# Kernel tuning notes

Hardware: AMD Instinct MI355X
Metric: run time of the kernel (lower is better)

## Reference

```python
import jax, jax.numpy as jnp
import numpy as np

B, N, INDIM, OUTDIM = 32, 128, 32, 64


def setup_inputs() -> dict:
    key = jax.random.key(0)
    k1, k2, k3, k4, k5, k6 = jax.random.split(key, 6)
    X = jax.random.normal(k1, (B, N, N, INDIM), dtype=jnp.float32)
    # variable subgraph sizes (irregular masking), at least 1 node per graph
    n_nodes = jnp.clip(jax.random.randint(k2, (B,), 0, N), 1, N).astype(jnp.int64)
    # MLP params (Linear + ReLU tail activation) for lin1 and lin2
    s = 1.0 / np.sqrt(INDIM)
    W1 = jax.random.uniform(k3, (INDIM, OUTDIM), jnp.float32, -s, s)
    b1 = jax.random.uniform(k4, (OUTDIM,), jnp.float32, -s, s)
    W2 = jax.random.uniform(k5, (INDIM, OUTDIM), jnp.float32, -s, s)
    b2 = jax.random.uniform(k6, (OUTDIM,), jnp.float32, -s, s)
    return {"X": X, "W1": W1, "b1": b1, "W2": W2, "b2": b2, "n_nodes": n_nodes}


def reference(X, W1, b1, W2, b2, n_nodes):
    # pairwise mask [B,N,N,1] from per-graph node counts (MaskedTensor mode 'DD')
    nm = jnp.arange(N)[None, :] < n_nodes[:, None]          # [B,N] node mask
    mask = (nm[:, :, None] & nm[:, None, :])[..., None].astype(X.dtype)  # [B,N,N,1]
    # tuplewiseapply of lin1 / lin2 (Linear + ReLU), zero-fill masked tuples
    X1 = jax.nn.relu(jnp.einsum('bijd,de->bije', X, W1) + b1) * mask  # [B,N,N,OUTDIM]
    X2 = jax.nn.relu(jnp.einsum('bijd,de->bije', X, W2) + b2) * mask
    # Op2FWL (aggr='sum'): per-channel batched matmul over node dim k
    out = jnp.einsum('bike,bkje->bije', X1, X2) * mask
    return out
```

## Files before the change

### kernel.cpp

```cpp
#include <hip/hip_runtime.h>

typedef unsigned short ushort_t;
typedef __attribute__((ext_vector_type(8))) __bf16 bf16x8;
typedef __attribute__((ext_vector_type(4))) float f32x4;


__device__ __forceinline__ ushort_t f32_to_bf16(float v) {
    unsigned ui = __float_as_uint(v);
    ui += 0x7fffu + ((ui >> 16) & 1u);
    return (ushort_t)(ui >> 16);
}

union FragU { bf16x8 f; ushort_t u[8]; };
union Pack4 { ushort_t us[4]; uint2 v; };

__global__ __launch_bounds__(256) void lin_mfma_kernel(
        const float* __restrict__ X,
        const float* __restrict__ W1, const float* __restrict__ b1v,
        const float* __restrict__ W2, const float* __restrict__ b2v,
        const int* __restrict__ n_nodes,
        ushort_t* __restrict__ X1t, ushort_t* __restrict__ X2t) {
    __shared__ ushort_t sO[64 * 136];
    const int blk = blockIdx.x;
    const int pass = blk >> 10;
    const int idx = blk & 1023;
    const int b = idx >> 5, rg = idx & 31;
    const int n = n_nodes[b];
    if (rg * 4 >= n) return;

    const float* W    = pass ? W2  : W1;
    const float* bias = pass ? b2v : b1v;
    ushort_t* Out     = pass ? X2t : X1t;
    const int rstride = pass ? 32 : 4096;
    const int tstride = pass ? 4096 : 32;

    const int u = threadIdx.x;
    const int w = u >> 6, l = u & 63;
    const int quad = l >> 4, lid = l & 15;

    FragU bfrag[4];
    float bia[4];
    #pragma unroll
    for (int ni = 0; ni < 4; ++ni) {
        const int e = ni * 16 + lid;
        #pragma unroll
        for (int j = 0; j < 8; ++j)
            bfrag[ni].u[j] = f32_to_bf16(W[(quad * 8 + j) * 64 + e]);
        bia[ni] = bias[e];
    }

    for (int q = 0; q < 4; ++q) {
        const int r = rg * 4 + q;
        if (r >= n) break;
        {
            const float* Xb = X + (size_t)b * 524288 + (size_t)r * rstride;
            #pragma unroll
            for (int s = 0; s < 2; ++s) {
                const int mt = w * 2 + s;
                const int t0b = mt * 16 + quad * 4;
                if (mt * 16 < n) {
                    const int m = mt * 16 + lid;
                    const float* xr = Xb + (size_t)m * tstride + quad * 8;
                    float4 x0 = *(const float4*)xr;
                    float4 x1 = *(const float4*)(xr + 4);
                    FragU af;
                    af.u[0] = f32_to_bf16(x0.x); af.u[1] = f32_to_bf16(x0.y);
                    af.u[2] = f32_to_bf16(x0.z); af.u[3] = f32_to_bf16(x0.w);
                    af.u[4] = f32_to_bf16(x1.x); af.u[5] = f32_to_bf16(x1.y);
                    af.u[6] = f32_to_bf16(x1.z); af.u[7] = f32_to_bf16(x1.w);
                    #pragma unroll
                    for (int ni = 0; ni < 4; ++ni) {
                        f32x4 acc = {};
                        acc = __builtin_amdgcn_mfma_f32_16x16x32_bf16(
                            af.f, bfrag[ni].f, acc, 0, 0, 0);
                        const int e = ni * 16 + lid;
                        Pack4 pk;
                        #pragma unroll
                        for (int rgi = 0; rgi < 4; ++rgi) {
                            const int t = t0b + rgi;
                            float v = (t < n) ? fmaxf(acc[rgi] + bia[ni], 0.f) : 0.f;
                            pk.us[rgi] = f32_to_bf16(v);
                        }
                        *(uint2*)(sO + e * 136 + t0b) = pk.v;
                    }
                } else {
                    Pack4 pk; pk.us[0] = pk.us[1] = pk.us[2] = pk.us[3] = 0;
                    #pragma unroll
                    for (int ni = 0; ni < 4; ++ni)
                        *(uint2*)(sO + (ni * 16 + lid) * 136 + t0b) = pk.v;
                }
            }
        }
        __syncthreads();
        {
            const int e = u >> 2, part = u & 3;
            if (part * 32 < n) {
                ushort_t* gO = Out + ((size_t)(b * 64 + e) * 128 + r) * 128 + part * 32;
                const ushort_t* sRow = sO + e * 136 + part * 32;
                #pragma unroll
                for (int c = 0; c < 4; ++c)
                    *(uint4*)(gO + c * 8) = *(const uint4*)(sRow + c * 8);
            }
        }
        __syncthreads();
    }
}

__global__ __launch_bounds__(256) void mm_kernel(
        const ushort_t* __restrict__ X1t, const ushort_t* __restrict__ X2t,
        ushort_t* __restrict__ Ct, const int* __restrict__ n_nodes) {
    __shared__ ushort_t sC[128 * 136];
    const int blk = blockIdx.x;
    const size_t plane = (size_t)blk * 16384;
    const int n = n_nodes[blk >> 6];
    const int kmax = (n + 31) & ~31;
    const ushort_t* Aj = X2t + plane;
    const ushort_t* Bi = X1t + plane;
    const int u = threadIdx.x;
    const int w = u >> 6, l = u & 63;
    const int quad = l >> 4, lid = l & 15;
    const int wj = (w >> 1) * 64, wi = (w & 1) * 64;
    const bool anyA = (wj < n), anyB = (wi < n);
    bool aAct[4], bAct[4];
    #pragma unroll
    for (int mj = 0; mj < 4; ++mj) aAct[mj] = (wj + mj * 16) < n;
    #pragma unroll
    for (int ni = 0; ni < 4; ++ni) bAct[ni] = (wi + ni * 16) < n;
    f32x4 acc[4][4] = {};

    for (int k0 = 0; k0 < kmax; k0 += 32) {
        bf16x8 af[4], bfr[4];
        #pragma unroll
        for (int mj = 0; mj < 4; ++mj)
            if (aAct[mj] && anyB)
                af[mj] = *(const bf16x8*)(Aj + (size_t)(wj + mj * 16 + lid) * 128 + k0 + quad * 8);
        #pragma unroll
        for (int ni = 0; ni < 4; ++ni)
            if (bAct[ni] && anyA)
                bfr[ni] = *(const bf16x8*)(Bi + (size_t)(wi + ni * 16 + lid) * 128 + k0 + quad * 8);
        #pragma unroll
        for (int mj = 0; mj < 4; ++mj)
            #pragma unroll
            for (int ni = 0; ni < 4; ++ni)
                if (aAct[mj] && bAct[ni])
                    acc[mj][ni] = __builtin_amdgcn_mfma_f32_16x16x32_bf16(
                        af[mj], bfr[ni], acc[mj][ni], 0, 0, 0);
    }

    #pragma unroll
    for (int mj = 0; mj < 4; ++mj)
        #pragma unroll
        for (int ni = 0; ni < 4; ++ni) {
            const int j0 = wj + mj * 16 + quad * 4;
            const int i  = wi + ni * 16 + lid;
            Pack4 pk;
            #pragma unroll
            for (int rg = 0; rg < 4; ++rg)
                pk.us[rg] = f32_to_bf16(acc[mj][ni][rg]);
            *(uint2*)(sC + i * 136 + j0) = pk.v;
        }
    __syncthreads();
    ushort_t* Cp = Ct + plane;
    #pragma unroll
    for (int it = 0; it < 8; ++it) {
        int idx = it * 256 + u;
        int i = idx >> 4, c = idx & 15;
        if (i < n && c * 8 < n)
            *(uint4*)(Cp + (size_t)idx * 8) = *(const uint4*)(sC + i * 136 + c * 8);
    }
}

__global__ __launch_bounds__(256) void tr_kernel(
        const ushort_t* __restrict__ Ct, float* __restrict__ out,
        const int* __restrict__ n_nodes) {
    __shared__ float sT[64 * 129];
    const int blk = blockIdx.x;
    const int b = blk >> 7, i = blk & 127;
    const int u = threadIdx.x;
    const int n = n_nodes[b];
    float* ob = out + ((size_t)b * 16384 + (size_t)i * 128) * 64;

    if (i >= n) {
        float4 z = {0.f, 0.f, 0.f, 0.f};
        #pragma unroll
        for (int it = 0; it < 8; ++it)
            *(float4*)(ob + (size_t)(it * 256 + u) * 4) = z;
        return;
    }

    const ushort_t* Cb = Ct + (size_t)b * 1048576 + (size_t)i * 128;
    #pragma unroll
    for (int it = 0; it < 4; ++it) {
        int idx = it * 256 + u;
        int e = idx >> 4, c = idx & 15;
        float* dst = sT + e * 129 + c * 8;
        const int rem = n - c * 8;
        if (rem >= 8) {
            uint4 v = *(const uint4*)(Cb + (size_t)e * 16384 + c * 8);
            dst[0] = __uint_as_float(v.x << 16);
            dst[1] = __uint_as_float(v.x & 0xffff0000u);
            dst[2] = __uint_as_float(v.y << 16);
            dst[3] = __uint_as_float(v.y & 0xffff0000u);
            dst[4] = __uint_as_float(v.z << 16);
            dst[5] = __uint_as_float(v.z & 0xffff0000u);
            dst[6] = __uint_as_float(v.w << 16);
            dst[7] = __uint_as_float(v.w & 0xffff0000u);
        } else if (rem > 0) {
            uint4 v = *(const uint4*)(Cb + (size_t)e * 16384 + c * 8);
            float tmp[8];
            tmp[0] = __uint_as_float(v.x << 16);
            tmp[1] = __uint_as_float(v.x & 0xffff0000u);
            tmp[2] = __uint_as_float(v.y << 16);
            tmp[3] = __uint_as_float(v.y & 0xffff0000u);
            tmp[4] = __uint_as_float(v.z << 16);
            tmp[5] = __uint_as_float(v.z & 0xffff0000u);
            tmp[6] = __uint_as_float(v.w << 16);
            tmp[7] = __uint_as_float(v.w & 0xffff0000u);
            #pragma unroll
            for (int t = 0; t < 8; ++t) dst[t] = (t < rem) ? tmp[t] : 0.f;
        } else {
            #pragma unroll
            for (int t = 0; t < 8; ++t) dst[t] = 0.f;
        }
    }
    __syncthreads();

    #pragma unroll
    for (int it = 0; it < 8; ++it) {
        int idx = it * 256 + u;
        int j = idx >> 4, e0 = (idx & 15) * 4;
        float4 vv;
        vv.x = sT[(e0 + 0) * 129 + j];
        vv.y = sT[(e0 + 1) * 129 + j];
        vv.z = sT[(e0 + 2) * 129 + j];
        vv.w = sT[(e0 + 3) * 129 + j];
        *(float4*)(ob + (size_t)idx * 4) = vv;
    }
}

extern "C" void kernel_launch(void* const* d_in, const int* in_sizes, int n_in,
                              void* d_out, int out_size, void* d_ws, size_t ws_size,
                              hipStream_t stream) {
    const float* X  = (const float*)d_in[0];
    const float* W1 = (const float*)d_in[1];
    const float* b1 = (const float*)d_in[2];
    const float* W2 = (const float*)d_in[3];
    const float* b2 = (const float*)d_in[4];
    const int* nn   = (const int*)d_in[5];
    float* out = (float*)d_out;

    ushort_t* X1t = (ushort_t*)d_ws;
    ushort_t* X2t = X1t + 33554432;
    ushort_t* Ct  = X1t;

    lin_mfma_kernel<<<2048, 256, 0, stream>>>(X, W1, b1, W2, b2, nn, X1t, X2t);
    mm_kernel<<<2048, 256, 0, stream>>>(X1t, X2t, Ct, nn);
    tr_kernel<<<4096, 256, 0, stream>>>(Ct, out, nn);
}
```

Measured before the change: 268.1 us.

## Tile linear kernel over 32x32 (i,j) blocks, computing both projections from one X tile

The linear stage now assigns each block a 32x32 (i,j) tile and a half of the output channels. Each block computes both the X1 and X2 projections from the same X tile, writing X2 transposed through shared memory. Before, X was read twice with a strided access pattern for the X2 pass. The aim is to read X contiguously and reuse it across both projections, at the cost of each X tile being read by two channel-half blocks and of scalar-granularity transposed LDS stores.

```diff
diff --git a/kernel.cpp b/kernel.cpp
--- a/kernel.cpp
+++ b/kernel.cpp
@@ -14,92 +14,105 @@
 union FragU { bf16x8 f; ushort_t u[8]; };
 union Pack4 { ushort_t us[4]; uint2 v; };
 
-__global__ __launch_bounds__(256) void lin_mfma_kernel(
+#define SYP 1036
+
+__global__ __launch_bounds__(256) void lin2_kernel(
         const float* __restrict__ X,
         const float* __restrict__ W1, const float* __restrict__ b1v,
         const float* __restrict__ W2, const float* __restrict__ b2v,
         const int* __restrict__ n_nodes,
         ushort_t* __restrict__ X1t, ushort_t* __restrict__ X2t) {
-    __shared__ ushort_t sO[64 * 136];
+    __shared__ ushort_t sY[32 * SYP];
     const int blk = blockIdx.x;
-    const int pass = blk >> 10;
-    const int idx = blk & 1023;
-    const int b = idx >> 5, rg = idx & 31;
+    const int b  = blk >> 5;
+    const int eh = (blk >> 4) & 1;
+    const int it = (blk >> 2) & 3, jt = blk & 3;
+    const int i0 = it * 32, j0 = jt * 32;
     const int n = n_nodes[b];
-    if (rg * 4 >= n) return;
-
-    const float* W    = pass ? W2  : W1;
-    const float* bias = pass ? b2v : b1v;
-    ushort_t* Out     = pass ? X2t : X1t;
-    const int rstride = pass ? 32 : 4096;
-    const int tstride = pass ? 4096 : 32;
-
+    if (i0 >= n || j0 >= n) return;
     const int u = threadIdx.x;
     const int w = u >> 6, l = u & 63;
     const int quad = l >> 4, lid = l & 15;
-
-    FragU bfrag[4];
-    float bia[4];
-    #pragma unroll
-    for (int ni = 0; ni < 4; ++ni) {
-        const int e = ni * 16 + lid;
-        #pragma unroll
-        for (int j = 0; j < 8; ++j)
-            bfrag[ni].u[j] = f32_to_bf16(W[(quad * 8 + j) * 64 + e]);
-        bia[ni] = bias[e];
-    }
-
-    for (int q = 0; q < 4; ++q) {
-        const int r = rg * 4 + q;
-        if (r >= n) break;
-        {
-            const float* Xb = X + (size_t)b * 524288 + (size_t)r * rstride;
-            #pragma unroll
-            for (int s = 0; s < 2; ++s) {
-                const int mt = w * 2 + s;
-                const int t0b = mt * 16 + quad * 4;
-                if (mt * 16 < n) {
-                    const int m = mt * 16 + lid;
-                    const float* xr = Xb + (size_t)m * tstride + quad * 8;
-                    float4 x0 = *(const float4*)xr;
-                    float4 x1 = *(const float4*)(xr + 4);
-                    FragU af;
-                    af.u[0] = f32_to_bf16(x0.x); af.u[1] = f32_to_bf16(x0.y);
-                    af.u[2] = f32_to_bf16(x0.z); af.u[3] = f32_to_bf16(x0.w);
-                    af.u[4] = f32_to_bf16(x1.x); af.u[5] = f32_to_bf16(x1.y);
-                    af.u[6] = f32_to_bf16(x1.z); af.u[7] = f32_to_bf16(x1.w);
-                    #pragma unroll
-                    for (int ni = 0; ni < 4; ++ni) {
-                        f32x4 acc = {};
-                        acc = __builtin_amdgcn_mfma_f32_16x16x32_bf16(
-                            af.f, bfrag[ni].f, acc, 0, 0, 0);
-                        const int e = ni * 16 + lid;
+    const int e0 = eh * 32;
+    const float* Xb = X + (size_t)b * 524288;
+
+    for (int p = 0; p < 2; ++p) {
+        const float* W    = p ? W2  : W1;
+        const float* bias = p ? b2v : b1v;
+        ushort_t* Out     = p ? X2t : X1t;
+        const int r0 = p ? j0 : i0;
+        const int c0 = p ? i0 : j0;
+
+        FragU bfrag[2];
+        float bia[2];
+        #pragma unroll
+        for (int ni = 0; ni < 2; ++ni) {
+            const int e = e0 + ni * 16 + lid;
+            #pragma unroll
+            for (int jj = 0; jj < 8; ++jj)
+                bfrag[ni].u[jj] = f32_to_bf16(W[(quad * 8 + jj) * 64 + e]);
+            bia[ni] = bias[e];
+        }
+
+        for (int mm = 0; mm < 16; ++mm) {
+            const int mt = w * 16 + mm;
+            const int il = mt >> 1, jl0 = (mt & 1) * 16;
+            const int gi = i0 + il;
+            if (gi < n) {
+                const float* xr = Xb + (size_t)gi * 4096
+                                     + (size_t)(j0 + jl0 + lid) * 32 + quad * 8;
+                float4 x0 = *(const float4*)xr;
+                float4 x1 = *(const float4*)(xr + 4);
+                FragU af;
+                af.u[0] = f32_to_bf16(x0.x); af.u[1] = f32_to_bf16(x0.y);
+                af.u[2] = f32_to_bf16(x0.z); af.u[3] = f32_to_bf16(x0.w);
+                af.u[4] = f32_to_bf16(x1.x); af.u[5] = f32_to_bf16(x1.y);
+                af.u[6] = f32_to_bf16(x1.z); af.u[7] = f32_to_bf16(x1.w);
+                #pragma unroll
+                for (int ni = 0; ni < 2; ++ni) {
+                    f32x4 acc = {};
+                    acc = __builtin_amdgcn_mfma_f32_16x16x32_bf16(
+                        af.f, bfrag[ni].f, acc, 0, 0, 0);
+                    const int el = ni * 16 + lid;
+                    if (p == 0) {
                         Pack4 pk;
                         #pragma unroll
-                        for (int rgi = 0; rgi < 4; ++rgi) {
-                            const int t = t0b + rgi;
-                            float v = (t < n) ? fmaxf(acc[rgi] + bia[ni], 0.f) : 0.f;
-                            pk.us[rgi] = f32_to_bf16(v);
+                        for (int rg = 0; rg < 4; ++rg) {
+                            const int gj = j0 + jl0 + quad * 4 + rg;
+                            float v = (gj < n) ? fmaxf(acc[rg] + bia[ni], 0.f) : 0.f;
+                            pk.us[rg] = f32_to_bf16(v);
                         }
-                        *(uint2*)(sO + e * 136 + t0b) = pk.v;
+                        *(uint2*)(sY + el * SYP + il * 32 + jl0 + quad * 4) = pk.v;
+                    } else {
+                        #pragma unroll
+                        for (int rg = 0; rg < 4; ++rg) {
+                            const int jl = jl0 + quad * 4 + rg;
+                            float v = ((j0 + jl) < n) ? fmaxf(acc[rg] + bia[ni], 0.f) : 0.f;
+                            sY[el * SYP + jl * 32 + il] = f32_to_bf16(v);
+                        }
                     }
-                } else {
-                    Pack4 pk; pk.us[0] = pk.us[1] = pk.us[2] = pk.us[3] = 0;
+                }
+            } else if (p == 1) {
+                #pragma unroll
+                for (int ni = 0; ni < 2; ++ni) {
+                    const int el = ni * 16 + lid;
                     #pragma unroll
-                    for (int ni = 0; ni < 4; ++ni)
-                        *(uint2*)(sO + (ni * 16 + lid) * 136 + t0b) = pk.v;
+                    for (int rg = 0; rg < 4; ++rg)
+                        sY[el * SYP + (jl0 + quad * 4 + rg) * 32 + il] = 0;
                 }
             }
         }
         __syncthreads();
+
         {
-            const int e = u >> 2, part = u & 3;
-            if (part * 32 < n) {
-                ushort_t* gO = Out + ((size_t)(b * 64 + e) * 128 + r) * 128 + part * 32;
-                const ushort_t* sRow = sO + e * 136 + part * 32;
-                #pragma unroll
-                for (int c = 0; c < 4; ++c)
-                    *(uint4*)(gO + c * 8) = *(const uint4*)(sRow + c * 8);
+            const int el = (u >> 2) & 31, part = u & 3, rhalf = u >> 7;
+            ushort_t* Ob = Out + ((size_t)(b * 64 + e0 + el) * 128 + r0) * 128
+                               + c0 + part * 8;
+            const ushort_t* Sb = sY + el * SYP + part * 8;
+            for (int rr = 0; rr < 16; ++rr) {
+                const int rl = rr * 2 + rhalf;
+                if (r0 + rl < n)
+                    *(uint4*)(Ob + (size_t)rl * 128) = *(const uint4*)(Sb + rl * 32);
             }
         }
         __syncthreads();
@@ -253,7 +266,7 @@
     ushort_t* X2t = X1t + 33554432;
     ushort_t* Ct  = X1t;
 
-    lin_mfma_kernel<<<2048, 256, 0, stream>>>(X, W1, b1, W2, b2, nn, X1t, X2t);
+    lin2_kernel<<<1024, 256, 0, stream>>>(X, W1, b1, W2, b2, nn, X1t, X2t);
     mm_kernel<<<2048, 256, 0, stream>>>(X1t, X2t, Ct, nn);
     tr_kernel<<<4096, 256, 0, stream>>>(Ct, out, nn);
 }
```

After: 299.4 us. 1.12x slower.

## Stage per-channel A/B planes in swizzled LDS before MFMA loop in mm_kernel

Applied to the files above, without the earlier changes.

The batched matmul kernel now loads each 128x128 bf16 plane of X1t and X2t once from global memory into shared memory, using an XOR swizzle, and bounds the copy by the active node count. MFMA fragments are then read from LDS instead of global memory, so the redundant global loads made by each warp are removed. The shared buffer is reused for the output staging after a barrier. The cost is 64KB of LDS per block, which may reduce occupancy, and an upfront load phase that is not overlapped with compute.

```diff
diff --git a/kernel.cpp b/kernel.cpp
--- a/kernel.cpp
+++ b/kernel.cpp
@@ -109,18 +109,35 @@
 __global__ __launch_bounds__(256) void mm_kernel(
         const ushort_t* __restrict__ X1t, const ushort_t* __restrict__ X2t,
         ushort_t* __restrict__ Ct, const int* __restrict__ n_nodes) {
-    __shared__ ushort_t sC[128 * 136];
+    __shared__ uint4 sMem4[4096];
     const int blk = blockIdx.x;
     const size_t plane = (size_t)blk * 16384;
     const int n = n_nodes[blk >> 6];
     const int kmax = (n + 31) & ~31;
+    const int rmax16 = (n + 15) >> 4;
+    const int cmax = kmax >> 3;
     const ushort_t* Aj = X2t + plane;
     const ushort_t* Bi = X1t + plane;
+    uint4* sA4 = sMem4;
+    uint4* sB4 = sMem4 + 2048;
     const int u = threadIdx.x;
     const int w = u >> 6, l = u & 63;
     const int quad = l >> 4, lid = l & 15;
+
+    {
+        const int rq = u >> 4, c = u & 15;
+        if (c < cmax) {
+            const int cs = c ^ (rq & 7);
+            for (int rb = 0; rb < rmax16; ++rb) {
+                const int r = rb * 16 + rq;
+                sA4[r * 16 + cs] = *(const uint4*)(Aj + (size_t)r * 128 + c * 8);
+                sB4[r * 16 + cs] = *(const uint4*)(Bi + (size_t)r * 128 + c * 8);
+            }
+        }
+    }
+    __syncthreads();
+
     const int wj = (w >> 1) * 64, wi = (w & 1) * 64;
-    const bool anyA = (wj < n), anyB = (wi < n);
     bool aAct[4], bAct[4];
     #pragma unroll
     for (int mj = 0; mj < 4; ++mj) aAct[mj] = (wj + mj * 16) < n;
@@ -128,16 +145,20 @@
     for (int ni = 0; ni < 4; ++ni) bAct[ni] = (wi + ni * 16) < n;
     f32x4 acc[4][4] = {};
 
+    const bf16x8* sAf = (const bf16x8*)sA4;
+    const bf16x8* sBf = (const bf16x8*)sB4;
+    const int lsw = lid & 7;
     for (int k0 = 0; k0 < kmax; k0 += 32) {
+        const int kb = k0 >> 3;
         bf16x8 af[4], bfr[4];
         #pragma unroll
         for (int mj = 0; mj < 4; ++mj)
-            if (aAct[mj] && anyB)
-                af[mj] = *(const bf16x8*)(Aj + (size_t)(wj + mj * 16 + lid) * 128 + k0 + quad * 8);
+            if (aAct[mj])
+                af[mj] = sAf[(wj + mj * 16 + lid) * 16 + ((kb + quad) ^ lsw)];
         #pragma unroll
         for (int ni = 0; ni < 4; ++ni)
-            if (bAct[ni] && anyA)
-                bfr[ni] = *(const bf16x8*)(Bi + (size_t)(wi + ni * 16 + lid) * 128 + k0 + quad * 8);
+            if (bAct[ni])
+                bfr[ni] = sBf[(wi + ni * 16 + lid) * 16 + ((kb + quad) ^ lsw)];
         #pragma unroll
         for (int mj = 0; mj < 4; ++mj)
             #pragma unroll
@@ -146,7 +167,9 @@
                     acc[mj][ni] = __builtin_amdgcn_mfma_f32_16x16x32_bf16(
                         af[mj], bfr[ni], acc[mj][ni], 0, 0, 0);
     }
-
+    __syncthreads();
+
+    ushort_t* sC = (ushort_t*)sMem4;
     #pragma unroll
     for (int mj = 0; mj < 4; ++mj)
         #pragma unroll
```

Measured after the change: 262.5 us. 2.1% less time.

## Stage mm operands through double-buffered LDS and use native bf16 conversion

Applied to the files above, without the earlier changes.

The batched matmul kernel now loads each 32-wide k-slice of both operands once per block into a padded, double-buffered shared-memory tile. Waves then read MFMA fragments from LDS instead of each wave fetching overlapping rows from global memory. This removes duplicate global loads at the cost of a barrier per k-step and more LDS use, and the output staging buffer now reuses the same LDS. The manual round-to-nearest bf16 bit trick is also replaced with the compiler's native float-to-bf16 cast, which may map to a hardware convert instruction.

```diff
diff --git a/kernel.cpp b/kernel.cpp
--- a/kernel.cpp
+++ b/kernel.cpp
@@ -5,14 +5,10 @@
 typedef __attribute__((ext_vector_type(4))) float f32x4;
 
 
-__device__ __forceinline__ ushort_t f32_to_bf16(float v) {
-    unsigned ui = __float_as_uint(v);
-    ui += 0x7fffu + ((ui >> 16) & 1u);
-    return (ushort_t)(ui >> 16);
-}
-
-union FragU { bf16x8 f; ushort_t u[8]; };
-union Pack4 { ushort_t us[4]; uint2 v; };
+__device__ __forceinline__ __bf16 cvt_bf16(float v) { return (__bf16)v; }
+
+union FragU  { bf16x8 f; __bf16 h[8]; };
+union Pack4  { __bf16 h[4]; uint2 v; };
 
 __global__ __launch_bounds__(256) void lin_mfma_kernel(
         const float* __restrict__ X,
@@ -45,7 +41,7 @@
         const int e = ni * 16 + lid;
         #pragma unroll
         for (int j = 0; j < 8; ++j)
-            bfrag[ni].u[j] = f32_to_bf16(W[(quad * 8 + j) * 64 + e]);
+            bfrag[ni].h[j] = cvt_bf16(W[(quad * 8 + j) * 64 + e]);
         bia[ni] = bias[e];
     }
 
@@ -64,10 +60,10 @@
                     float4 x0 = *(const float4*)xr;
                     float4 x1 = *(const float4*)(xr + 4);
                     FragU af;
-                    af.u[0] = f32_to_bf16(x0.x); af.u[1] = f32_to_bf16(x0.y);
-                    af.u[2] = f32_to_bf16(x0.z); af.u[3] = f32_to_bf16(x0.w);
-                    af.u[4] = f32_to_bf16(x1.x); af.u[5] = f32_to_bf16(x1.y);
-                    af.u[6] = f32_to_bf16(x1.z); af.u[7] = f32_to_bf16(x1.w);
+                    af.h[0] = cvt_bf16(x0.x); af.h[1] = cvt_bf16(x0.y);
+                    af.h[2] = cvt_bf16(x0.z); af.h[3] = cvt_bf16(x0.w);
+                    af.h[4] = cvt_bf16(x1.x); af.h[5] = cvt_bf16(x1.y);
+                    af.h[6] = cvt_bf16(x1.z); af.h[7] = cvt_bf16(x1.w);
                     #pragma unroll
                     for (int ni = 0; ni < 4; ++ni) {
                         f32x4 acc = {};
@@ -79,12 +75,13 @@
                         for (int rgi = 0; rgi < 4; ++rgi) {
                             const int t = t0b + rgi;
                             float v = (t < n) ? fmaxf(acc[rgi] + bia[ni], 0.f) : 0.f;
-                            pk.us[rgi] = f32_to_bf16(v);
+                            pk.h[rgi] = cvt_bf16(v);
                         }
                         *(uint2*)(sO + e * 136 + t0b) = pk.v;
                     }
                 } else {
-                    Pack4 pk; pk.us[0] = pk.us[1] = pk.us[2] = pk.us[3] = 0;
+                    Pack4 pk;
+                    pk.h[0] = pk.h[1] = pk.h[2] = pk.h[3] = cvt_bf16(0.f);
                     #pragma unroll
                     for (int ni = 0; ni < 4; ++ni)
                         *(uint2*)(sO + (ni * 16 + lid) * 136 + t0b) = pk.v;
@@ -106,21 +103,40 @@
     }
 }
 
+#define MMP 5
 __global__ __launch_bounds__(256) void mm_kernel(
         const ushort_t* __restrict__ X1t, const ushort_t* __restrict__ X2t,
         ushort_t* __restrict__ Ct, const int* __restrict__ n_nodes) {
-    __shared__ ushort_t sC[128 * 136];
+    __shared__ uint4 sS[2 * 2 * 128 * MMP];
     const int blk = blockIdx.x;
     const size_t plane = (size_t)blk * 16384;
     const int n = n_nodes[blk >> 6];
     const int kmax = (n + 31) & ~31;
+    const int T = kmax >> 5;
+    const int R = (n + 15) & ~15;
     const ushort_t* Aj = X2t + plane;
     const ushort_t* Bi = X1t + plane;
     const int u = threadIdx.x;
     const int w = u >> 6, l = u & 63;
     const int quad = l >> 4, lid = l & 15;
+    const int srow = u >> 2, sc = u & 3;
+
+    auto STAGE = [&](int t, int bsel) {
+        uint4* dA = sS + bsel * (2 * 128 * MMP);
+        uint4* dB = dA + 128 * MMP;
+        const ushort_t* gA = Aj + t * 32 + sc * 8;
+        const ushort_t* gB = Bi + t * 32 + sc * 8;
+        #pragma unroll
+        for (int p = 0; p < 2; ++p) {
+            const int r = p * 64 + srow;
+            if (r < R) {
+                dA[r * MMP + sc] = *(const uint4*)(gA + (size_t)r * 128);
+                dB[r * MMP + sc] = *(const uint4*)(gB + (size_t)r * 128);
+            }
+        }
+    };
+
     const int wj = (w >> 1) * 64, wi = (w & 1) * 64;
-    const bool anyA = (wj < n), anyB = (wi < n);
     bool aAct[4], bAct[4];
     #pragma unroll
     for (int mj = 0; mj < 4; ++mj) aAct[mj] = (wj + mj * 16) < n;
@@ -128,16 +144,21 @@
     for (int ni = 0; ni < 4; ++ni) bAct[ni] = (wi + ni * 16) < n;
     f32x4 acc[4][4] = {};
 
-    for (int k0 = 0; k0 < kmax; k0 += 32) {
+    STAGE(0, 0);
+    __syncthreads();
+    for (int t = 0; t < T; ++t) {
+        if (t + 1 < T) STAGE(t + 1, (t + 1) & 1);
+        const uint4* bA = sS + (t & 1) * (2 * 128 * MMP);
+        const uint4* bB = bA + 128 * MMP;
         bf16x8 af[4], bfr[4];
         #pragma unroll
         for (int mj = 0; mj < 4; ++mj)
-            if (aAct[mj] && anyB)
-                af[mj] = *(const bf16x8*)(Aj + (size_t)(wj + mj * 16 + lid) * 128 + k0 + quad * 8);
+            if (aAct[mj])
+                af[mj] = *(const bf16x8*)&bA[(wj + mj * 16 + lid) * MMP + quad];
         #pragma unroll
         for (int ni = 0; ni < 4; ++ni)
-            if (bAct[ni] && anyA)
-                bfr[ni] = *(const bf16x8*)(Bi + (size_t)(wi + ni * 16 + lid) * 128 + k0 + quad * 8);
+            if (bAct[ni])
+                bfr[ni] = *(const bf16x8*)&bB[(wi + ni * 16 + lid) * MMP + quad];
         #pragma unroll
         for (int mj = 0; mj < 4; ++mj)
             #pragma unroll
@@ -145,8 +166,10 @@
                 if (aAct[mj] && bAct[ni])
                     acc[mj][ni] = __builtin_amdgcn_mfma_f32_16x16x32_bf16(
                         af[mj], bfr[ni], acc[mj][ni], 0, 0, 0);
-    }
-
+        __syncthreads();
+    }
+
+    ushort_t* sC = (ushort_t*)sS;
     #pragma unroll
     for (int mj = 0; mj < 4; ++mj)
         #pragma unroll
@@ -156,7 +179,7 @@
             Pack4 pk;
             #pragma unroll
             for (int rg = 0; rg < 4; ++rg)
-                pk.us[rg] = f32_to_bf16(acc[mj][ni][rg]);
+                pk.h[rg] = cvt_bf16(acc[mj][ni][rg]);
             *(uint2*)(sC + i * 136 + j0) = pk.v;
         }
     __syncthreads();
```

Result: faster. 260.4 us (-2.8%).
